# Performance work log

Measured on AMD Instinct MI355X. Metric: run time of the kernel, lower is better.

Reference implementation:

```python
import jax, jax.numpy as jnp
import numpy as np
import math

B, S, HID, NH = 2, 2048, 1024, 16
HD = HID // NH  # head_dim = 64
TEMPERATURE = 1.0


def setup_inputs() -> dict:
    key = jax.random.key(0)
    ks = jax.random.split(key, 6)
    w = lambda k: (jax.random.normal(k, (HID, HID), dtype=jnp.float32) * 0.02)
    return {
        "hidden_states": jax.random.normal(ks[0], (B, S, HID), dtype=jnp.float32),
        "attention_mask": jnp.ones((B, S), dtype=jnp.float32),
        "Wq": w(ks[1]), "bq": jnp.zeros((HID,), jnp.float32),
        "Wk": w(ks[2]), "bk": jnp.zeros((HID,), jnp.float32),
        "Wv": w(ks[3]), "bv": jnp.zeros((HID,), jnp.float32),
        "Wo": w(ks[4]), "bo": jnp.zeros((HID,), jnp.float32),
    }


def reference(hidden_states, attention_mask, Wq, bq, Wk, bk, Wv, bv, Wo, bo):
    b, s, hid = hidden_states.shape
    heads = lambda x: x.reshape(b, s, NH, HD).transpose(0, 2, 1, 3)  # [b,h,s,d]

    q = heads(hidden_states @ Wq.T + bq)
    k = heads(hidden_states @ Wk.T + bk)
    v = heads(hidden_states @ Wv.T + bv)

    # padding mask applied multiplicatively to k and v
    m = attention_mask[:, None, :, None]  # [b,1,s,1]
    k = k * m
    v = v * m

    # auxiliary Hopfield state: k^T @ v per head -> [b,h,d,d]
    state = jnp.einsum("bhsd,bhse->bhde", k, v)

    # energy / scores
    energy = jnp.einsum("bhqd,bhkd->bhqk", q, k) / (TEMPERATURE * math.sqrt(HD))
    causal = jnp.triu(jnp.ones((s, s), dtype=bool), k=1)  # True above diagonal
    energy = jnp.where(causal[None, None], -jnp.inf, energy)
    energy = jnp.where(attention_mask[:, None, None, :] == 0, -jnp.inf, energy)

    attn = jax.nn.softmax(energy, axis=-1)
    out = jnp.einsum("bhqk,bhkd->bhqd", attn, v)
    out = out.transpose(0, 2, 1, 3).reshape(b, s, hid)
    out = out @ Wo.T + bo
    return out, state
```

## Files before the change

kernel.cpp:

```cpp
#include <hip/hip_runtime.h>
#include <hip/hip_bf16.h>

#define B_ 2
#define S_ 2048
#define HID_ 1024
#define NH_ 16
#define HD_ 64
#define MTOK (B_*S_)
#define LDQKV 3072
#define SCALE_LOG2E 0.18033688011112043f

typedef __attribute__((ext_vector_type(8))) __bf16 bf16x8;
typedef __attribute__((ext_vector_type(4))) __bf16 bf16x4;
typedef __attribute__((ext_vector_type(4))) float f32x4;

__device__ __forceinline__ void gl16(__bf16* lds, const __bf16* g) {
  __builtin_amdgcn_global_load_lds(
      (const __attribute__((address_space(1))) void*)g,
      (__attribute__((address_space(3))) void*)lds, 16, 0, 0);
}

__device__ __forceinline__ int gswz(int row) { return ((row ^ (row >> 2)) & 3) << 4; }

__global__ __launch_bounds__(256) void cast_all(
    const float* __restrict__ X,
    const float* __restrict__ Wq, const float* __restrict__ Wk,
    const float* __restrict__ Wv, const float* __restrict__ Wo,
    __bf16* __restrict__ Xb, __bf16* __restrict__ Wqkvb, __bf16* __restrict__ Wob)
{
  int i = blockIdx.x * 256 + threadIdx.x;
  const float* src; __bf16* dst; int j;
  if (i < (1 << 20))              { src = X;  dst = Xb;                 j = i; }
  else if (i < (1<<20)+(1<<18))   { src = Wq; dst = Wqkvb;              j = i - (1<<20); }
  else if (i < (1<<20)+(2<<18))   { src = Wk; dst = Wqkvb + (1<<20);    j = i - (1<<20) - (1<<18); }
  else if (i < (1<<20)+(3<<18))   { src = Wv; dst = Wqkvb + (2<<20);    j = i - (1<<20) - (2<<18); }
  else                            { src = Wo; dst = Wob;                j = i - (1<<20) - (3<<18); }
  float4 v = reinterpret_cast<const float4*>(src)[j];
  bf16x4 o;
  o[0] = (__bf16)v.x; o[1] = (__bf16)v.y; o[2] = (__bf16)v.z; o[3] = (__bf16)v.w;
  reinterpret_cast<bf16x4*>(dst)[j] = o;
}

__global__ __launch_bounds__(256) void gemm_qkv(
    const __bf16* __restrict__ A, const __bf16* __restrict__ W,
    const float* __restrict__ bq, const float* __restrict__ bk,
    const float* __restrict__ bv, const float* __restrict__ mask,
    __bf16* __restrict__ C)
{
  __shared__ __bf16 SM[24576];
  const int t = threadIdx.x;
  const int m0 = blockIdx.y * 128;
  const int n0 = blockIdx.x * 128;
  const int lane = t & 63;
  const int w = t >> 6;
  const int wr = (w >> 1) * 64;
  const int wc = (w & 1) * 64;
  const int fr = lane & 15;
  const int kg = lane >> 4;

  f32x4 acc[4][4];
  #pragma unroll
  for (int i = 0; i < 4; i++)
    #pragma unroll
    for (int j = 0; j < 4; j++) acc[i][j] = (f32x4)0.f;

  const int srow = w * 16 + (lane >> 2);
  const int scolb = ((lane & 3) * 16) ^ gswz(srow);
  const __bf16* ap0 = A + (size_t)(m0 + srow) * HID_ + (scolb >> 1);
  const __bf16* ap1 = A + (size_t)(m0 + 64 + srow) * HID_ + (scolb >> 1);
  const __bf16* wp0 = W + (size_t)(n0 + srow) * HID_ + (scolb >> 1);
  const __bf16* wp1 = W + (size_t)(n0 + 64 + srow) * HID_ + (scolb >> 1);

  #define STAGE3(buf, koff) { \
    __bf16* ab = SM + (buf) * 4096; \
    __bf16* bb = SM + 12288 + (buf) * 4096; \
    gl16(ab + w * 512, ap0 + (koff)); \
    gl16(ab + 2048 + w * 512, ap1 + (koff)); \
    gl16(bb + w * 512, wp0 + (koff)); \
    gl16(bb + 2048 + w * 512, wp1 + (koff)); }

  STAGE3(0, 0);
  STAGE3(1, 32);
  int bc = 0, bp2 = 2;
  for (int step = 0; step < 32; ++step) {
    if (step + 1 < 32) { asm volatile("s_waitcnt vmcnt(4)" ::: "memory"); }
    else               { asm volatile("s_waitcnt vmcnt(0)" ::: "memory"); }
    __builtin_amdgcn_sched_barrier(0);
    __builtin_amdgcn_s_barrier();
    if (step + 2 < 32) STAGE3(bp2, (step + 2) * 32);

    const __bf16* ab = SM + bc * 4096;
    const __bf16* bb = SM + 12288 + bc * 4096;
    bf16x8 af[4], bf[4];
    #pragma unroll
    for (int m = 0; m < 4; m++) {
      int row = wr + m*16 + fr;
      af[m] = *(const bf16x8*)((const char*)ab + row * 64 + ((kg * 16) ^ gswz(row)));
    }
    #pragma unroll
    for (int n = 0; n < 4; n++) {
      int row = wc + n*16 + fr;
      bf[n] = *(const bf16x8*)((const char*)bb + row * 64 + ((kg * 16) ^ gswz(row)));
    }
    #pragma unroll
    for (int m = 0; m < 4; m++)
      #pragma unroll
      for (int n = 0; n < 4; n++)
        acc[m][n] = __builtin_amdgcn_mfma_f32_16x16x32_bf16(af[m], bf[n], acc[m][n], 0, 0, 0);

    bc = (bc == 2) ? 0 : bc + 1;
    bp2 = (bp2 == 2) ? 0 : bp2 + 1;
  }

  const int region = n0 >> 10;
  const float* bias = region == 0 ? bq : (region == 1 ? bk : bv);
  const int nloc = n0 & 1023;

  #pragma unroll
  for (int m = 0; m < 4; m++) {
    #pragma unroll
    for (int r = 0; r < 4; r++) {
      int row = m0 + wr + m*16 + kg*4 + r;
      float rs = region ? mask[row] : SCALE_LOG2E;
      #pragma unroll
      for (int n = 0; n < 4; n++) {
        int c = wc + n*16 + fr;
        C[(size_t)row * LDQKV + n0 + c] = (__bf16)((acc[m][n][r] + bias[nloc + c]) * rs);
      }
    }
  }
}

__global__ __launch_bounds__(256) void transpose_kv(
    const __bf16* __restrict__ Kin, const __bf16* __restrict__ Vin,
    __bf16* __restrict__ Kt, __bf16* __restrict__ Vt)
{
  __shared__ __bf16 tile[64][68];
  const int tok0 = blockIdx.x * 64;
  const int f0 = blockIdx.y * 64;
  const __bf16* in = blockIdx.z ? Vin : Kin;
  __bf16* out = blockIdx.z ? Vt : Kt;
  const int t = threadIdx.x;
  const int r = t >> 2;
  const int c0 = (t & 3) * 16;
  const __bf16* src = in + (size_t)(tok0 + r) * LDQKV + f0 + c0;
  *(bf16x8*)&tile[r][c0]     = *(const bf16x8*)src;
  *(bf16x8*)&tile[r][c0 + 8] = *(const bf16x8*)(src + 8);
  __syncthreads();
  bf16x8 o0, o1;
  #pragma unroll
  for (int j = 0; j < 8; j++) { o0[j] = tile[c0 + j][r]; o1[j] = tile[c0 + 8 + j][r]; }
  __bf16* dst = out + (size_t)(f0 + r) * MTOK + tok0 + c0;
  *(bf16x8*)dst = o0;
  *(bf16x8*)(dst + 8) = o1;
}

__global__ __launch_bounds__(256) void gemm_o(
    const __bf16* __restrict__ A, const __bf16* __restrict__ W,
    const float* __restrict__ bias, const float* __restrict__ part,
    float* __restrict__ C)
{
  if (blockIdx.y >= 32) {
    const int bl = blockIdx.x + (blockIdx.y - 32) * 8;
    const int tid = bl * 256 + threadIdx.x;
    float* outState = C + (size_t)MTOK * HID_;
    #pragma unroll 4
    for (int e = 0; e < 32; e++) {
      int i = e * 4096 + tid;
      int bh = i >> 12, de = i & 4095;
      float s = 0.f;
      #pragma unroll
      for (int sc = 0; sc < 8; sc++) s += part[(size_t)((bh << 3) + sc) * 4096 + de];
      outState[i] = s;
    }
    return;
  }

  __shared__ __bf16 SM[24576];
  const int t = threadIdx.x;
  const int m0 = blockIdx.y * 128;
  const int n0 = blockIdx.x * 128;
  const int lane = t & 63;
  const int w = t >> 6;
  const int wr = (w >> 1) * 64;
  const int wc = (w & 1) * 64;
  const int fr = lane & 15;
  const int kg = lane >> 4;

  f32x4 acc[4][4];
  #pragma unroll
  for (int i = 0; i < 4; i++)
    #pragma unroll
    for (int j = 0; j < 4; j++) acc[i][j] = (f32x4)0.f;

  const int srow = w * 16 + (lane >> 2);
  const int scolb = ((lane & 3) * 16) ^ gswz(srow);
  const __bf16* ap0 = A + (size_t)(m0 + srow) * HID_ + (scolb >> 1);
  const __bf16* ap1 = A + (size_t)(m0 + 64 + srow) * HID_ + (scolb >> 1);
  const __bf16* wp0 = W + (size_t)(n0 + srow) * HID_ + (scolb >> 1);
  const __bf16* wp1 = W + (size_t)(n0 + 64 + srow) * HID_ + (scolb >> 1);

  STAGE3(0, 0);
  STAGE3(1, 32);
  int bc = 0, bp2 = 2;
  for (int step = 0; step < 32; ++step) {
    if (step + 1 < 32) { asm volatile("s_waitcnt vmcnt(4)" ::: "memory"); }
    else               { asm volatile("s_waitcnt vmcnt(0)" ::: "memory"); }
    __builtin_amdgcn_sched_barrier(0);
    __builtin_amdgcn_s_barrier();
    if (step + 2 < 32) STAGE3(bp2, (step + 2) * 32);

    const __bf16* ab = SM + bc * 4096;
    const __bf16* bb = SM + 12288 + bc * 4096;
    bf16x8 af[4], bf[4];
    #pragma unroll
    for (int m = 0; m < 4; m++) {
      int row = wr + m*16 + fr;
      af[m] = *(const bf16x8*)((const char*)ab + row * 64 + ((kg * 16) ^ gswz(row)));
    }
    #pragma unroll
    for (int n = 0; n < 4; n++) {
      int row = wc + n*16 + fr;
      bf[n] = *(const bf16x8*)((const char*)bb + row * 64 + ((kg * 16) ^ gswz(row)));
    }
    #pragma unroll
    for (int m = 0; m < 4; m++)
      #pragma unroll
      for (int n = 0; n < 4; n++)
        acc[m][n] = __builtin_amdgcn_mfma_f32_16x16x32_bf16(af[m], bf[n], acc[m][n], 0, 0, 0);

    bc = (bc == 2) ? 0 : bc + 1;
    bp2 = (bp2 == 2) ? 0 : bp2 + 1;
  }

  #pragma unroll
  for (int m = 0; m < 4; m++) {
    #pragma unroll
    for (int r = 0; r < 4; r++) {
      int row = m0 + wr + m*16 + kg*4 + r;
      #pragma unroll
      for (int n = 0; n < 4; n++) {
        int col = n0 + wc + n*16 + fr;
        C[(size_t)row * HID_ + col] = acc[m][n][r] + bias[col];
      }
    }
  }
}

__device__ __forceinline__ bf16x8 ld_swz(const __bf16* base, int row, int xb) {
  return *(const bf16x8*)((const char*)base + row * 128 + (xb ^ ((row & 7) << 4)));
}
__device__ __forceinline__ void st_swz16(__bf16* base, int row, int colbyte, __bf16 v) {
  *(__bf16*)((char*)base + row * 128 + (colbyte ^ ((row & 7) << 4))) = v;
}
__device__ __forceinline__ bf16x8 ld_swz256(const __bf16* base, int row, int xb) {
  return *(const bf16x8*)((const char*)base + row * 256 + (xb ^ ((row & 7) << 4)));
}

__device__ __forceinline__ void attn_tile(
    const __bf16* __restrict__ ks, const __bf16* __restrict__ vs,
    const bool (&okm)[4], __bf16* __restrict__ pw,
    const bf16x8 (&qa)[2], f32x4 (&acc)[4], f32x4& accl,
    const bf16x8 ones, int q0w, int kt, int fc, int kg)
{
  f32x4 s[4];
  #pragma unroll
  for (int n = 0; n < 4; n++) s[n] = (f32x4)0.f;
  __builtin_amdgcn_s_setprio(1);
  #pragma unroll
  for (int kd = 0; kd < 2; kd++)
    #pragma unroll
    for (int n = 0; n < 4; n++) {
      bf16x8 kf = ld_swz(ks, n * 16 + fc, kd * 64 + kg * 16);
      s[n] = __builtin_amdgcn_mfma_f32_16x16x32_bf16(qa[kd], kf, s[n], 0, 0, 0);
    }
  __builtin_amdgcn_s_setprio(0);

  const int g4 = kg * 4;
  const bool fullt = (kt * 64 + 63 <= q0w);
  if (fullt) {
    #pragma unroll
    for (int r = 0; r < 4; r++)
      #pragma unroll
      for (int n = 0; n < 4; n++) {
        float p = okm[n] ? __builtin_amdgcn_exp2f(s[n][r]) : 0.f;
        st_swz16(pw, g4 + r, (n * 16 + fc) * 2, (__bf16)p);
      }
  } else {
    #pragma unroll
    for (int r = 0; r < 4; r++) {
      const int qg = q0w + g4 + r;
      #pragma unroll
      for (int n = 0; n < 4; n++) {
        bool ok = okm[n] && (kt * 64 + n * 16 + fc <= qg);
        float p = ok ? __builtin_amdgcn_exp2f(s[n][r]) : 0.f;
        st_swz16(pw, g4 + r, (n * 16 + fc) * 2, (__bf16)p);
      }
    }
  }

  __builtin_amdgcn_s_setprio(1);
  #pragma unroll
  for (int kc = 0; kc < 2; kc++) {
    bf16x8 pf = ld_swz(pw, fc, kc * 64 + kg * 16);
    accl = __builtin_amdgcn_mfma_f32_16x16x32_bf16(pf, ones, accl, 0, 0, 0);
    #pragma unroll
    for (int n = 0; n < 4; n++) {
      bf16x8 vf = ld_swz(vs, n * 16 + fc, kc * 64 + kg * 16);
      acc[n] = __builtin_amdgcn_mfma_f32_16x16x32_bf16(pf, vf, acc[n], 0, 0, 0);
    }
  }
  __builtin_amdgcn_s_setprio(0);
}

__global__ __launch_bounds__(256) void flash_state(
    const __bf16* __restrict__ Q, const __bf16* __restrict__ K,
    const __bf16* __restrict__ Vt, const float* __restrict__ mask,
    __bf16* __restrict__ O, const __bf16* __restrict__ Kt,
    float* __restrict__ part)
{
  __shared__ __bf16 Ks[2][64 * 64];
  __shared__ __bf16 Vs[2][64 * 64];
  __shared__ __bf16 Ps[4][16 * 64];

  const int t = threadIdx.x;
  const int w = t >> 6;
  const int lane = t & 63;
  const int fc = lane & 15;
  const int kg = lane >> 4;

  if (blockIdx.y >= 32) {
    const int bh = blockIdx.x, sc = blockIdx.y - 32;
    const int b = bh >> 4, h = bh & 15;
    __bf16* Kl = &Ks[0][0];
    __bf16* Vl = &Vs[0][0];
    const int rloc = lane >> 4;
    const int cb = (lane & 15) * 16;

    f32x4 acc[4];
    #pragma unroll
    for (int n = 0; n < 4; n++) acc[n] = (f32x4)0.f;

    for (int ch = 0; ch < 2; ch++) {
      const size_t colbase = (size_t)b * S_ + sc * 256 + ch * 128;
      __syncthreads();
      #pragma unroll
      for (int c = 0; c < 4; c++) {
        int row = w * 16 + c * 4 + rloc;
        int scol = (cb ^ ((row & 7) << 4)) >> 1;
        gl16(&Kl[(w * 16 + c * 4) * 128], Kt + (size_t)(h * HD_ + row) * MTOK + colbase + scol);
        gl16(&Vl[(w * 16 + c * 4) * 128], Vt + (size_t)(h * HD_ + row) * MTOK + colbase + scol);
      }
      __syncthreads();

      #pragma unroll
      for (int ks = 0; ks < 4; ks++) {
        bf16x8 af = ld_swz256(Kl, w * 16 + fc, ks * 64 + kg * 16);
        #pragma unroll
        for (int n = 0; n < 4; n++) {
          bf16x8 bfr = ld_swz256(Vl, n * 16 + fc, ks * 64 + kg * 16);
          acc[n] = __builtin_amdgcn_mfma_f32_16x16x32_bf16(af, bfr, acc[n], 0, 0, 0);
        }
      }
    }

    float* dst = part + ((size_t)((bh << 3) + sc) << 12);
    #pragma unroll
    for (int n = 0; n < 4; n++)
      #pragma unroll
      for (int r = 0; r < 4; r++)
        dst[(w * 16 + kg * 4 + r) * 64 + n * 16 + fc] = acc[n][r];
    return;
  }

  const int bh = blockIdx.x;
  const int ya = (int)blockIdx.y & 7;
  const int yg = (int)blockIdx.y >> 3;
  const int qt = (yg == 0) ? 31 - ya : (yg == 1) ? 16 + ya
               : (yg == 2) ? 15 - ya : ya;
  const int b = bh >> 4, h = bh & 15;
  const int g4 = kg * 4;

  const int q0w = qt * 64 + w * 16;
  const size_t tokbase = (size_t)b * S_;

  const int rr = lane >> 3;
  const int cswz = ((lane & 7) ^ rr) * 8;
  const int ktmax = qt;

  bf16x8 qa[2];
  {
    const __bf16* qp = Q + (tokbase + q0w + fc) * LDQKV + h * HD_;
    qa[0] = *(const bf16x8*)(qp + kg * 8);
    qa[1] = *(const bf16x8*)(qp + 32 + kg * 8);
  }

  const float* mp = mask + tokbase + fc;
  float mnxt[4];
  #pragma unroll
  for (int n = 0; n < 4; n++) mnxt[n] = mp[n * 16];

  const __bf16* kp0 = K + (tokbase + (size_t)(w * 16 + rr)) * LDQKV + h * HD_ + cswz;
  const __bf16* kp1 = kp0 + (size_t)8 * LDQKV;
  const __bf16* vp0 = Vt + (size_t)(h * HD_ + w * 16 + rr) * MTOK + tokbase + cswz;
  const __bf16* vp1 = vp0 + (size_t)8 * MTOK;

  gl16(&Ks[0][(w * 16) * 64],     kp0);
  gl16(&Ks[0][(w * 16 + 8) * 64], kp1);
  gl16(&Vs[0][(w * 16) * 64],     vp0);
  gl16(&Vs[0][(w * 16 + 8) * 64], vp1);
  kp0 += (size_t)64 * LDQKV; kp1 += (size_t)64 * LDQKV;
  vp0 += 64; vp1 += 64;

  bf16x8 ones;
  #pragma unroll
  for (int j = 0; j < 8; j++) ones[j] = (__bf16)1.f;

  f32x4 acc[4], accl;
  #pragma unroll
  for (int n = 0; n < 4; n++) acc[n] = (f32x4)0.f;
  accl = (f32x4)0.f;

  __bf16* pw = &Ps[w][0];

  for (int kt = 0; kt <= ktmax; ++kt) {
    const int cur = kt & 1;
    float mcur[4];
    #pragma unroll
    for (int n = 0; n < 4; n++) mcur[n] = mnxt[n];

    if (kt < ktmax) {
      #pragma unroll
      for (int n = 0; n < 4; n++) mnxt[n] = mp[(kt + 1) * 64 + n * 16];
      const int nxt = cur ^ 1;
      gl16(&Ks[nxt][(w * 16) * 64],     kp0);
      gl16(&Ks[nxt][(w * 16 + 8) * 64], kp1);
      gl16(&Vs[nxt][(w * 16) * 64],     vp0);
      gl16(&Vs[nxt][(w * 16 + 8) * 64], vp1);
      kp0 += (size_t)64 * LDQKV; kp1 += (size_t)64 * LDQKV;
      vp0 += 64; vp1 += 64;
      asm volatile("s_waitcnt vmcnt(8)" ::: "memory");
    } else {
      asm volatile("s_waitcnt vmcnt(0)" ::: "memory");
    }
    __builtin_amdgcn_sched_barrier(0);
    __builtin_amdgcn_s_barrier();

    bool okm[4];
    #pragma unroll
    for (int n = 0; n < 4; n++) okm[n] = (mcur[n] != 0.f);

    attn_tile(&Ks[cur][0], &Vs[cur][0], okm, pw, qa, acc, accl, ones, q0w, kt, fc, kg);

    __builtin_amdgcn_s_barrier();
  }

  #pragma unroll
  for (int r = 0; r < 4; r++) {
    float inv = accl[r] > 0.f ? 1.f / accl[r] : 0.f;
    __bf16* op = O + (tokbase + q0w + g4 + r) * HID_ + h * HD_;
    #pragma unroll
    for (int n = 0; n < 4; n++)
      op[n * 16 + fc] = (__bf16)(acc[n][r] * inv);
  }
}

extern "C" void kernel_launch(void* const* d_in, const int* in_sizes, int n_in,
                              void* d_out, int out_size, void* d_ws, size_t ws_size,
                              hipStream_t stream)
{
  const float* hs   = (const float*)d_in[0];
  const float* mask = (const float*)d_in[1];
  const float* Wq   = (const float*)d_in[2];
  const float* bq   = (const float*)d_in[3];
  const float* Wk   = (const float*)d_in[4];
  const float* bk   = (const float*)d_in[5];
  const float* Wv   = (const float*)d_in[6];
  const float* bv   = (const float*)d_in[7];
  const float* Wo   = (const float*)d_in[8];
  const float* bo   = (const float*)d_in[9];
  float* out = (float*)d_out;

  char* ws = (char*)d_ws;
  __bf16* Wqkvb = (__bf16*)(ws);
  __bf16* Wob   = (__bf16*)(ws + (6u  << 20));
  __bf16* Xb    = (__bf16*)(ws + (8u  << 20));
  __bf16* QKV   = (__bf16*)(ws + (16u << 20));
  __bf16* Ob    = (__bf16*)(ws + (40u << 20));
  __bf16* Ktg   = (__bf16*)(ws + (48u << 20));

  cast_all<<<8192, 256, 0, stream>>>(hs, Wq, Wk, Wv, Wo, Xb, Wqkvb, Wob);

  gemm_qkv<<<dim3(LDQKV / 128, MTOK / 128), 256, 0, stream>>>(
      Xb, Wqkvb, bq, bk, bv, mask, QKV);

  __bf16* Vtg = Xb;
  transpose_kv<<<dim3(MTOK / 64, HID_ / 64, 2), 256, 0, stream>>>(
      QKV + 1024, QKV + 2048, Ktg, Vtg);

  float* part = (float*)Wqkvb;

  flash_state<<<dim3(B_ * NH_, 40), 256, 0, stream>>>(
      QKV, QKV + 1024, Vtg, mask, Ob, Ktg, part);

  gemm_o<<<dim3(HID_ / 128, 34), 256, 0, stream>>>(Ob, Wob, bo, part, out);
}
```

Measured before the change: 122.0 us.

## Single-buffer V tile and issue its load after each attention step

Switches the attention loop from double-buffering both K and V to double-buffering only K, with a single V buffer. The next V tile is loaded after the trailing barrier of each iteration, and the shared arrays are merged into one SMEM array. This cuts LDS use from 40KB to 32KB per block, which could allow more resident blocks. In exchange, V loads have less time to hide their latency before the next iteration's wait, which may expose memory stalls.

```diff
diff --git a/kernel.cpp b/kernel.cpp
--- a/kernel.cpp
+++ b/kernel.cpp
@@ -319,9 +319,7 @@
     __bf16* __restrict__ O, const __bf16* __restrict__ Kt,
     float* __restrict__ part)
 {
-  __shared__ __bf16 Ks[2][64 * 64];
-  __shared__ __bf16 Vs[2][64 * 64];
-  __shared__ __bf16 Ps[4][16 * 64];
+  __shared__ __bf16 SMEM[16384];
 
   const int t = threadIdx.x;
   const int w = t >> 6;
@@ -332,8 +330,8 @@
   if (blockIdx.y >= 32) {
     const int bh = blockIdx.x, sc = blockIdx.y - 32;
     const int b = bh >> 4, h = bh & 15;
-    __bf16* Kl = &Ks[0][0];
-    __bf16* Vl = &Vs[0][0];
+    __bf16* Kl = &SMEM[0];
+    __bf16* Vl = &SMEM[8192];
     const int rloc = lane >> 4;
     const int cb = (lane & 15) * 16;
 
@@ -388,6 +386,9 @@
   const int cswz = ((lane & 7) ^ rr) * 8;
   const int ktmax = qt;
 
+  __bf16* Vsb = &SMEM[8192];
+  __bf16* pw = &SMEM[12288 + w * 1024];
+
   bf16x8 qa[2];
   {
     const __bf16* qp = Q + (tokbase + q0w + fc) * LDQKV + h * HD_;
@@ -395,22 +396,22 @@
     qa[1] = *(const bf16x8*)(qp + 32 + kg * 8);
   }
 
-  const float* mp = mask + tokbase + fc;
-  float mnxt[4];
-  #pragma unroll
-  for (int n = 0; n < 4; n++) mnxt[n] = mp[n * 16];
-
   const __bf16* kp0 = K + (tokbase + (size_t)(w * 16 + rr)) * LDQKV + h * HD_ + cswz;
   const __bf16* kp1 = kp0 + (size_t)8 * LDQKV;
   const __bf16* vp0 = Vt + (size_t)(h * HD_ + w * 16 + rr) * MTOK + tokbase + cswz;
   const __bf16* vp1 = vp0 + (size_t)8 * MTOK;
 
-  gl16(&Ks[0][(w * 16) * 64],     kp0);
-  gl16(&Ks[0][(w * 16 + 8) * 64], kp1);
-  gl16(&Vs[0][(w * 16) * 64],     vp0);
-  gl16(&Vs[0][(w * 16 + 8) * 64], vp1);
+  gl16(&SMEM[(w * 16) * 64],     kp0);
+  gl16(&SMEM[(w * 16 + 8) * 64], kp1);
   kp0 += (size_t)64 * LDQKV; kp1 += (size_t)64 * LDQKV;
+  gl16(&Vsb[(w * 16) * 64],     vp0);
+  gl16(&Vsb[(w * 16 + 8) * 64], vp1);
   vp0 += 64; vp1 += 64;
+
+  const float* mp = mask + tokbase + fc;
+  float mnxt[4];
+  #pragma unroll
+  for (int n = 0; n < 4; n++) mnxt[n] = mp[n * 16];
 
   bf16x8 ones;
   #pragma unroll
@@ -421,10 +422,7 @@
   for (int n = 0; n < 4; n++) acc[n] = (f32x4)0.f;
   accl = (f32x4)0.f;
 
-  __bf16* pw = &Ps[w][0];
-
   for (int kt = 0; kt <= ktmax; ++kt) {
-    const int cur = kt & 1;
     float mcur[4];
     #pragma unroll
     for (int n = 0; n < 4; n++) mcur[n] = mnxt[n];
@@ -432,14 +430,11 @@
     if (kt < ktmax) {
       #pragma unroll
       for (int n = 0; n < 4; n++) mnxt[n] = mp[(kt + 1) * 64 + n * 16];
-      const int nxt = cur ^ 1;
-      gl16(&Ks[nxt][(w * 16) * 64],     kp0);
-      gl16(&Ks[nxt][(w * 16 + 8) * 64], kp1);
-      gl16(&Vs[nxt][(w * 16) * 64],     vp0);
-      gl16(&Vs[nxt][(w * 16 + 8) * 64], vp1);
+      __bf16* kb = &SMEM[((kt + 1) & 1) * 4096];
+      gl16(&kb[(w * 16) * 64],     kp0);
+      gl16(&kb[(w * 16 + 8) * 64], kp1);
       kp0 += (size_t)64 * LDQKV; kp1 += (size_t)64 * LDQKV;
-      vp0 += 64; vp1 += 64;
-      asm volatile("s_waitcnt vmcnt(8)" ::: "memory");
+      asm volatile("s_waitcnt vmcnt(6)" ::: "memory");
     } else {
       asm volatile("s_waitcnt vmcnt(0)" ::: "memory");
     }
@@ -450,9 +445,15 @@
     #pragma unroll
     for (int n = 0; n < 4; n++) okm[n] = (mcur[n] != 0.f);
 
-    attn_tile(&Ks[cur][0], &Vs[cur][0], okm, pw, qa, acc, accl, ones, q0w, kt, fc, kg);
+    attn_tile(&SMEM[(kt & 1) * 4096], Vsb, okm, pw, qa, acc, accl, ones, q0w, kt, fc, kg);
 
     __builtin_amdgcn_s_barrier();
+
+    if (kt < ktmax) {
+      gl16(&Vsb[(w * 16) * 64],     vp0);
+      gl16(&Vsb[(w * 16 + 8) * 64], vp1);
+      vp0 += 64; vp1 += 64;
+    }
   }
 
   #pragma unroll
```

New measurement: 120.4 us. Within noise of the previous version (-1.3%).
